# Kernel tuning notes

Hardware: AMD Instinct MI355X
Metric: run time of the kernel (lower is better)

## Reference

```python
import jax, jax.numpy as jnp
import numpy as np
from math import sqrt

EMBED = 768
HEADS = 12
EPS = 1e-12  # torch F.normalize eps


def setup_inputs() -> dict:
    key = jax.random.key(0)
    ks = jax.random.split(key, 9)
    B, N, E = 8, 4096, EMBED
    s = 1.0 / np.sqrt(E)
    x = jax.random.normal(ks[0], (B, N, E), dtype=jnp.float32)
    Wq = jax.random.normal(ks[1], (E, E), dtype=jnp.float32) * s
    bq = jnp.zeros((E,), dtype=jnp.float32)
    Wk = jax.random.normal(ks[2], (E, E), dtype=jnp.float32) * s
    bk = jnp.zeros((E,), dtype=jnp.float32)
    Wv = jax.random.normal(ks[3], (E, E), dtype=jnp.float32) * s
    bv = jnp.zeros((E,), dtype=jnp.float32)
    Wo = jax.random.normal(ks[4], (E, E), dtype=jnp.float32) * s
    bo = jnp.zeros((E,), dtype=jnp.float32)
    return {"x": x, "Wq": Wq, "bq": bq, "Wk": Wk, "bk": bk,
            "Wv": Wv, "bv": bv, "Wo": Wo, "bo": bo}


def _l2norm_tokens(t):
    # F.normalize(p=2, dim=1): normalize over the token (n) axis
    nrm = jnp.sqrt(jnp.sum(t * t, axis=1, keepdims=True))
    return t / jnp.maximum(nrm, EPS)


def reference(x, Wq, bq, Wk, bk, Wv, bv, Wo, bo):
    B, N, E = x.shape
    h = HEADS
    e = E // h
    q = (x @ Wq + bq).reshape(B, N, h, e)
    k = (x @ Wk + bk).reshape(B, N, h, e)
    v = (x @ Wv + bv).reshape(B, N, h, e)
    q = _l2norm_tokens(q)
    k = _l2norm_tokens(k)
    # cross-covariance attention over channel dim: [b, e, h, e]
    energy = jnp.einsum('bnhe,bnhq->behq', q, k)
    attn = jax.nn.softmax(energy, axis=-1) / sqrt(E)
    out = jnp.einsum('behq,bnhe->bnhq', attn, v)  # [b, n, h, e]
    out = out.reshape(B, N, E)
    return out @ Wo + bo
```

## Files before the change

### kernel.cpp

```cpp
#include <hip/hip_runtime.h>
#include <hip/hip_bf16.h>

typedef short bf16x8 __attribute__((ext_vector_type(8)));
typedef unsigned short u16x8 __attribute__((ext_vector_type(8)));
typedef unsigned short us4 __attribute__((ext_vector_type(4)));
typedef float f32x4 __attribute__((ext_vector_type(4)));
using bf16 = __hip_bfloat16;

#define EMB 768
#define NHEAD 12
#define BATCH 8
#define NTOK 4096
#define BNTOK 32768

__device__ __forceinline__ float b2f(unsigned short u) {
    union { unsigned int i; float f; } x; x.i = ((unsigned int)u) << 16; return x.f;
}
__device__ __forceinline__ unsigned short f2bu(float f) {
    bf16 h = __float2bfloat16(f);
    return *reinterpret_cast<unsigned short*>(&h);
}

__device__ __forceinline__ void gload_lds16(const void* g, void* l) {
    __builtin_amdgcn_global_load_lds(
        (const __attribute__((address_space(1))) unsigned int*)g,
        (__attribute__((address_space(3))) unsigned int*)l,
        16, 0, 0);
}

__global__ __launch_bounds__(256) void cast_x_kernel(const float* __restrict__ x,
                                                     bf16* __restrict__ xb, int n8) {
    int i = blockIdx.x * blockDim.x + threadIdx.x;
    if (i >= n8) return;
    const float4* xv = (const float4*)x;
    float4 a = xv[i * 2], b = xv[i * 2 + 1];
    u16x8 o;
    o[0] = f2bu(a.x); o[1] = f2bu(a.y); o[2] = f2bu(a.z); o[3] = f2bu(a.w);
    o[4] = f2bu(b.x); o[5] = f2bu(b.y); o[6] = f2bu(b.z); o[7] = f2bu(b.w);
    ((u16x8*)xb)[i] = o;
}

__global__ __launch_bounds__(256) void prep_w_kernel(
    const float* __restrict__ Wq, const float* __restrict__ Wk,
    const float* __restrict__ Wv, const float* __restrict__ Wo,
    const float* __restrict__ bq, const float* __restrict__ bk, const float* __restrict__ bv,
    bf16* __restrict__ WqkvT, bf16* __restrict__ WoT, float* __restrict__ bqkv) {
    const int NQKV = 2304 * 768, NO = 768 * 768;
    int i = blockIdx.x * blockDim.x + threadIdx.x;
    if (i < NQKV) {
        int nrow = i / 768, k = i % 768;
        const float* W = (nrow < 768) ? Wq : (nrow < 1536 ? Wk : Wv);
        int c = nrow % 768;
        WqkvT[i] = __float2bfloat16(W[k * 768 + c]);
    } else if (i < NQKV + NO) {
        int j = i - NQKV; int nrow = j / 768, k = j % 768;
        WoT[j] = __float2bfloat16(Wo[k * 768 + nrow]);
    } else if (i < NQKV + NO + 2304) {
        int j = i - NQKV - NO;
        bqkv[j] = (j < 768) ? bq[j] : (j < 1536 ? bk[j - 768] : bv[j - 1536]);
    }
}

template <int MODE>
__global__ __launch_bounds__(512, 1) void gemm256(
    const bf16* __restrict__ A, const bf16* __restrict__ BT,
    bf16* __restrict__ QT, bf16* __restrict__ KT, bf16* __restrict__ V,
    const float* __restrict__ bias,
    float* __restrict__ Cout, const float* __restrict__ bo) {
    __shared__ char lds[131072];
    const int NKT = 12;
    const int tid = threadIdx.x;
    const int lane = tid & 63, wid = tid >> 6;
    const int wm = wid >> 2, wn = wid & 3;
    const int lrow = lane & 15, lk = lane >> 4;

    int nwg = gridDim.x * gridDim.y;
    int bid = blockIdx.y * gridDim.x + blockIdx.x;
    int swz = (bid & 7) * (nwg >> 3) + (bid >> 3);
    int bx = swz % gridDim.x, by = swz / gridDim.x;
    const int m0 = by * 256, n0 = bx * 256;

    const bf16* bt = BT + (MODE == 1 ? (size_t)(m0 >> 12) * 589824 : 0);

    const int srow = wid * 16 + lrow;
    const int scol = ((lane >> 4) & 3) << 3;

    f32x4 acc[8][4] = {};

#define STAGE(tbuf, isb, skh, sktv) do {                                           \
    int skt_ = (sktv); if (skt_ >= NKT) skt_ = NKT - 1;                            \
    const bf16* gp_ = ((isb) ? bt + (size_t)(n0 + srow) * 768                      \
                             : A  + (size_t)(m0 + srow) * 768)                     \
                      + skt_ * 64 + (skh) * 32 + scol;                             \
    char* lp_ = lds + (tbuf) * 65536 + (isb) * 32768 + (skh) * 16384 + wid * 1024; \
    gload_lds16(gp_, lp_);                                                         \
    gload_lds16(gp_ + (size_t)128 * 768, lp_ + 8192);                              \
} while (0)

#define LOADB(cbuf, KH) do {                                                       \
    const char* bb_ = lds + (cbuf) * 65536 + 32768 + (KH) * 16384;                 \
    _Pragma("unroll") for (int ni = 0; ni < 4; ++ni)                               \
        bre[ni] = *(const bf16x8*)(bb_ + (wn * 4 + ni) * 1024 + lane * 16);        \
} while (0)

#define COMPUTE(cbuf, KH, CM) do {                                                 \
    const char* ab_ = lds + (cbuf) * 65536 + (KH) * 16384;                         \
    bf16x8 af_[4];                                                                 \
    _Pragma("unroll") for (int mi = 0; mi < 4; ++mi)                               \
        af_[mi] = *(const bf16x8*)(ab_ + (wm * 8 + (CM) * 4 + mi) * 1024 + lane * 16); \
    __builtin_amdgcn_s_setprio(1);                                                 \
    _Pragma("unroll") for (int mi = 0; mi < 4; ++mi)                               \
    _Pragma("unroll") for (int ni = 0; ni < 4; ++ni)                               \
        acc[(CM) * 4 + mi][ni] = __builtin_amdgcn_mfma_f32_16x16x32_bf16(          \
            af_[mi], bre[ni], acc[(CM) * 4 + mi][ni], 0, 0, 0);                    \
    __builtin_amdgcn_s_setprio(0);                                                 \
} while (0)

#define VMC8 asm volatile("s_waitcnt vmcnt(8)" ::: "memory")
#define BAR  __builtin_amdgcn_s_barrier()

    bf16x8 bre[4];

    STAGE(0, 0, 0, 0);
    STAGE(0, 1, 0, 0);
    STAGE(0, 0, 1, 0);
    STAGE(0, 1, 1, 0);
    STAGE(1, 0, 0, 1);
    STAGE(1, 1, 0, 1);
    VMC8; BAR;

    for (int i = 0; i < NKT; ++i) {
        const int cb = i & 1, nb = cb ^ 1;
        STAGE(nb, 0, 1, i + 1); LOADB(cb, 0); COMPUTE(cb, 0, 0); BAR;
        STAGE(nb, 1, 1, i + 1); COMPUTE(cb, 0, 1); VMC8; BAR;
        STAGE(cb, 0, 0, i + 2); LOADB(cb, 1); COMPUTE(cb, 1, 0); BAR;
        STAGE(cb, 1, 0, i + 2); COMPUTE(cb, 1, 1); VMC8; BAR;
    }

#undef STAGE
#undef LOADB
#undef COMPUTE
#undef VMC8
#undef BAR

    if (MODE == 0) {
        const int which = n0 / 768;
        if (which < 2) {
            bf16* T = (which == 0) ? QT : KT;
            const int b = m0 >> 12;
            const int tb = (m0 & 4095) + wm * 128 + lk * 4;
#pragma unroll
            for (int ri = 0; ri < 8; ++ri)
#pragma unroll
                for (int ni = 0; ni < 4; ++ni) {
                    int gcol = n0 + wn * 64 + ni * 16 + lrow;
                    int chan = gcol - which * 768;
                    float bia = bias[gcol];
                    int tokl = tb + ri * 16;
                    us4 pk;
                    pk[0] = f2bu(acc[ri][ni][0] + bia);
                    pk[1] = f2bu(acc[ri][ni][1] + bia);
                    pk[2] = f2bu(acc[ri][ni][2] + bia);
                    pk[3] = f2bu(acc[ri][ni][3] + bia);
                    *(us4*)&T[((size_t)b * 768 + chan) * 4096 + tokl] = pk;
                }
        } else {
#pragma unroll
            for (int ri = 0; ri < 8; ++ri)
#pragma unroll
                for (int ni = 0; ni < 4; ++ni) {
                    int gcol = n0 + wn * 64 + ni * 16 + lrow;
                    int chan = gcol - 1536;
                    float bia = bias[gcol];
                    size_t r0 = (size_t)(m0 + wm * 128 + ri * 16 + lk * 4);
#pragma unroll
                    for (int r = 0; r < 4; ++r)
                        V[(r0 + r) * 768 + chan] = __float2bfloat16(acc[ri][ni][r] + bia);
                }
        }
    } else {
#pragma unroll
        for (int ri = 0; ri < 8; ++ri)
#pragma unroll
            for (int ni = 0; ni < 4; ++ni) {
                int col = n0 + wn * 64 + ni * 16 + lrow;
                float bia = bo[col];
                size_t r0 = (size_t)(m0 + wm * 128 + ri * 16 + lk * 4);
#pragma unroll
                for (int r = 0; r < 4; ++r)
                    Cout[(r0 + r) * 768 + col] = acc[ri][ni][r] + bia;
            }
    }
}

__global__ __launch_bounds__(256) void gram_mfma_kernel(
    const bf16* __restrict__ QT, const bf16* __restrict__ KT,
    float* __restrict__ G, float* __restrict__ ssq, float* __restrict__ ssk) {
    const int kc = blockIdx.x, bh = blockIdx.y;
    const int b = bh / NHEAD, h = bh % NHEAD;
    const int tid = threadIdx.x, lane = tid & 63, w = tid >> 6;
    const int lrow = lane & 15, lk = lane >> 4;
    const int t0 = kc * 512 + w * 128;

    f32x4 acc[4][4] = {};
    float sqp[4] = {}, skp[4] = {};
    const size_t qbase = ((size_t)b * 768 + h * 64) * 4096;

#pragma unroll
    for (int kk = 0; kk < 4; ++kk) {
        bf16x8 a[4], bb[4];
#pragma unroll
        for (int mi = 0; mi < 4; ++mi)
            a[mi] = *(const bf16x8*)(QT + qbase + (size_t)(mi * 16 + lrow) * 4096 +
                                     t0 + kk * 32 + lk * 8);
#pragma unroll
        for (int ni = 0; ni < 4; ++ni)
            bb[ni] = *(const bf16x8*)(KT + qbase + (size_t)(ni * 16 + lrow) * 4096 +
                                      t0 + kk * 32 + lk * 8);
#pragma unroll
        for (int mi = 0; mi < 4; ++mi) {
#pragma unroll
            for (int j = 0; j < 8; ++j) {
                float qv = b2f((unsigned short)a[mi][j]);
                float kv = b2f((unsigned short)bb[mi][j]);
                sqp[mi] = fmaf(qv, qv, sqp[mi]);
                skp[mi] = fmaf(kv, kv, skp[mi]);
            }
        }
#pragma unroll
        for (int mi = 0; mi < 4; ++mi)
#pragma unroll
            for (int ni = 0; ni < 4; ++ni)
                acc[mi][ni] = __builtin_amdgcn_mfma_f32_16x16x32_bf16(a[mi], bb[ni], acc[mi][ni], 0, 0, 0);
    }

#pragma unroll
    for (int mi = 0; mi < 4; ++mi) {
        float vq = sqp[mi], vk = skp[mi];
        vq += __shfl_down(vq, 32); vq += __shfl_down(vq, 16);
        vk += __shfl_down(vk, 32); vk += __shfl_down(vk, 16);
        if (lane < 16) {
            atomicAdd(&ssq[b * 768 + h * 64 + mi * 16 + lrow], vq);
            atomicAdd(&ssk[b * 768 + h * 64 + mi * 16 + lrow], vk);
        }
    }

    float* g = G + (size_t)bh * 4096;
#pragma unroll
    for (int mi = 0; mi < 4; ++mi)
#pragma unroll
        for (int ni = 0; ni < 4; ++ni)
#pragma unroll
            for (int r = 0; r < 4; ++r) {
                int e = mi * 16 + lk * 4 + r;
                int j = ni * 16 + lrow;
                atomicAdd(&g[e * 64 + j], acc[mi][ni][r]);
            }
}

__global__ __launch_bounds__(64) void softmax_kernel(
    const float* __restrict__ G, const float* __restrict__ ssq, const float* __restrict__ ssk,
    bf16* __restrict__ attnA) {
    int bh = blockIdx.x; int b = bh / NHEAD, h = bh % NHEAD;
    int e = threadIdx.x;
    const float* g = G + (size_t)bh * 4096 + e * 64;
    float nq = fmaxf(sqrtf(ssq[b * 768 + h * 64 + e]), 1e-12f);
    float row[64];
    float mx = -1e30f;
#pragma unroll
    for (int j = 0; j < 64; ++j) {
        float nk = fmaxf(sqrtf(ssk[b * 768 + h * 64 + j]), 1e-12f);
        float en = g[j] / (nq * nk);
        row[j] = en;
        mx = fmaxf(mx, en);
    }
    float s = 0.f;
#pragma unroll
    for (int j = 0; j < 64; ++j) { row[j] = __expf(row[j] - mx); s += row[j]; }
    float inv = 0.036084391824351615f / s;
#pragma unroll
    for (int j = 0; j < 64; ++j)
        attnA[(size_t)bh * 4096 + e * 64 + j] = __float2bfloat16(row[j] * inv);
}

__global__ __launch_bounds__(256) void wtilde_kernel(
    const bf16* __restrict__ WoT, const bf16* __restrict__ attnA,
    bf16* __restrict__ WtT) {
    const int ns = blockIdx.x, bh = blockIdx.y;
    const int b = bh / NHEAD, h = bh % NHEAD;
    const int tid = threadIdx.x, lane = tid & 63, w = tid >> 6;
    const int lrow = lane & 15, lk = lane >> 4;
    const int nbase = ns * 192 + w * 48;

    f32x4 acc[3][4] = {};
#pragma unroll
    for (int kk = 0; kk < 2; ++kk) {
        bf16x8 a[3], bb[4];
#pragma unroll
        for (int mi = 0; mi < 3; ++mi)
            a[mi] = *(const bf16x8*)(WoT + (size_t)(nbase + mi * 16 + lrow) * 768 +
                                     h * 64 + kk * 32 + lk * 8);
#pragma unroll
        for (int ni = 0; ni < 4; ++ni)
            bb[ni] = *(const bf16x8*)(attnA + (size_t)bh * 4096 +
                                      (ni * 16 + lrow) * 64 + kk * 32 + lk * 8);
#pragma unroll
        for (int mi = 0; mi < 3; ++mi)
#pragma unroll
            for (int ni = 0; ni < 4; ++ni)
                acc[mi][ni] = __builtin_amdgcn_mfma_f32_16x16x32_bf16(a[mi], bb[ni], acc[mi][ni], 0, 0, 0);
    }
#pragma unroll
    for (int mi = 0; mi < 3; ++mi)
#pragma unroll
        for (int ni = 0; ni < 4; ++ni)
#pragma unroll
            for (int r = 0; r < 4; ++r) {
                int n = nbase + mi * 16 + lk * 4 + r;
                int e = ni * 16 + lrow;
                WtT[((size_t)b * 768 + n) * 768 + h * 64 + e] = __float2bfloat16(acc[mi][ni][r]);
            }
}

extern "C" void kernel_launch(void* const* d_in, const int* in_sizes, int n_in,
                              void* d_out, int out_size, void* d_ws, size_t ws_size,
                              hipStream_t stream) {
    const float* x  = (const float*)d_in[0];
    const float* Wq = (const float*)d_in[1];
    const float* bq = (const float*)d_in[2];
    const float* Wk = (const float*)d_in[3];
    const float* bk = (const float*)d_in[4];
    const float* Wv = (const float*)d_in[5];
    const float* bv = (const float*)d_in[6];
    const float* Wo = (const float*)d_in[7];
    const float* bo = (const float*)d_in[8];
    float* out = (float*)d_out;

    char* ws = (char*)d_ws;
    bf16*  xb    = (bf16*)(ws + 0);
    bf16*  WqkvT = (bf16*)(ws + 50331648);
    bf16*  WoT   = (bf16*)(ws + 53870592);
    float* bqkv  = (float*)(ws + 55050240);
    bf16*  QT    = (bf16*)(ws + 55059456);
    bf16*  KT    = (bf16*)(ws + 105391104);
    bf16*  Vb    = (bf16*)(ws + 155722752);
    float* ssq   = (float*)(ws + 206054400);
    float* ssk   = (float*)(ws + 206078976);
    float* G     = (float*)(ws + 206103552);
    bf16*  attnA = (bf16*)(ws + 207676416);
    bf16*  WtT   = xb;

    hipMemsetAsync(ws + 206054400, 0, 24576 + 24576 + 1572864, stream);

    cast_x_kernel<<<12288, 256, 0, stream>>>(x, xb, BNTOK * EMB / 8);
    prep_w_kernel<<<9225, 256, 0, stream>>>(Wq, Wk, Wv, Wo, bq, bk, bv, WqkvT, WoT, bqkv);

    gemm256<0><<<dim3(9, 128), 512, 0, stream>>>(xb, WqkvT, QT, KT, Vb, bqkv, nullptr, nullptr);

    gram_mfma_kernel<<<dim3(8, 96), 256, 0, stream>>>(QT, KT, G, ssq, ssk);
    softmax_kernel<<<96, 64, 0, stream>>>(G, ssq, ssk, attnA);
    wtilde_kernel<<<dim3(4, 96), 256, 0, stream>>>(WoT, attnA, WtT);

    gemm256<1><<<dim3(3, 128), 512, 0, stream>>>(Vb, WtT, nullptr, nullptr, nullptr, nullptr, out, bo);
}
```

Measured before the change: 357.2 us.

## Restructure GEMM main loop staging order and stage Q/K transposed epilogue through LDS

The main loop is reorganised into phases that read A and B fragments from LDS, issue the next global-to-LDS stage, then barrier, wait on LDS and run the MFMAs. It changes the prefetch order and depth (vmcnt 8 to 10, with one more stage issued in the prologue). The Q/K transposed epilogue now writes bias-added bf16 tiles into LDS and then emits 16-byte coalesced row stores, instead of scattered 8-byte stores. This trades extra barriers and LDS traffic for better memory coalescing and more load/compute overlap.

```diff
diff --git a/kernel.cpp b/kernel.cpp
--- a/kernel.cpp
+++ b/kernel.cpp
@@ -97,50 +97,53 @@
     gload_lds16(gp_ + (size_t)128 * 768, lp_ + 8192);                              \
 } while (0)
 
-#define LOADB(cbuf, KH) do {                                                       \
-    const char* bb_ = lds + (cbuf) * 65536 + 32768 + (KH) * 16384;                 \
-    _Pragma("unroll") for (int ni = 0; ni < 4; ++ni)                               \
-        bre[ni] = *(const bf16x8*)(bb_ + (wn * 4 + ni) * 1024 + lane * 16);        \
-} while (0)
-
-#define COMPUTE(cbuf, KH, CM) do {                                                 \
+#define VMC10 asm volatile("s_waitcnt vmcnt(10)" ::: "memory")
+#define BAR   __builtin_amdgcn_s_barrier()
+
+#define PH(cbuf, KH, CM, RB, STG, DOV) do {                                        \
     const char* ab_ = lds + (cbuf) * 65536 + (KH) * 16384;                         \
-    bf16x8 af_[4];                                                                 \
     _Pragma("unroll") for (int mi = 0; mi < 4; ++mi)                               \
-        af_[mi] = *(const bf16x8*)(ab_ + (wm * 8 + (CM) * 4 + mi) * 1024 + lane * 16); \
+        afr[mi] = *(const bf16x8*)(ab_ + (wm * 8 + (CM) * 4 + mi) * 1024 + lane * 16); \
+    if (RB) {                                                                      \
+        const char* bb_ = ab_ + 32768;                                             \
+        _Pragma("unroll") for (int ni = 0; ni < 4; ++ni)                           \
+            bfr[ni] = *(const bf16x8*)(bb_ + (wn * 4 + ni) * 1024 + lane * 16);    \
+    }                                                                              \
+    STG;                                                                           \
+    BAR;                                                                           \
+    asm volatile("s_waitcnt lgkmcnt(0)" ::: "memory");                             \
     __builtin_amdgcn_s_setprio(1);                                                 \
     _Pragma("unroll") for (int mi = 0; mi < 4; ++mi)                               \
     _Pragma("unroll") for (int ni = 0; ni < 4; ++ni)                               \
         acc[(CM) * 4 + mi][ni] = __builtin_amdgcn_mfma_f32_16x16x32_bf16(          \
-            af_[mi], bre[ni], acc[(CM) * 4 + mi][ni], 0, 0, 0);                    \
+            afr[mi], bfr[ni], acc[(CM) * 4 + mi][ni], 0, 0, 0);                    \
     __builtin_amdgcn_s_setprio(0);                                                 \
+    if (DOV) VMC10;                                                                \
+    BAR;                                                                           \
 } while (0)
 
-#define VMC8 asm volatile("s_waitcnt vmcnt(8)" ::: "memory")
-#define BAR  __builtin_amdgcn_s_barrier()
-
-    bf16x8 bre[4];
-
+    bf16x8 afr[4], bfr[4];
+
+    STAGE(0, 1, 0, 0);
     STAGE(0, 0, 0, 0);
-    STAGE(0, 1, 0, 0);
+    STAGE(0, 1, 1, 0);
     STAGE(0, 0, 1, 0);
-    STAGE(0, 1, 1, 0);
+    STAGE(1, 1, 0, 1);
     STAGE(1, 0, 0, 1);
-    STAGE(1, 1, 0, 1);
-    VMC8; BAR;
+    STAGE(1, 1, 1, 1);
+    VMC10; BAR;
 
     for (int i = 0; i < NKT; ++i) {
         const int cb = i & 1, nb = cb ^ 1;
-        STAGE(nb, 0, 1, i + 1); LOADB(cb, 0); COMPUTE(cb, 0, 0); BAR;
-        STAGE(nb, 1, 1, i + 1); COMPUTE(cb, 0, 1); VMC8; BAR;
-        STAGE(cb, 0, 0, i + 2); LOADB(cb, 1); COMPUTE(cb, 1, 0); BAR;
-        STAGE(cb, 1, 0, i + 2); COMPUTE(cb, 1, 1); VMC8; BAR;
+        PH(cb, 0, 0, 1, STAGE(nb, 0, 1, i + 1), 0);
+        PH(cb, 0, 1, 0, STAGE(cb, 1, 0, i + 2), 1);
+        PH(cb, 1, 0, 1, STAGE(cb, 0, 0, i + 2), 0);
+        PH(cb, 1, 1, 0, STAGE(cb, 1, 1, i + 2), 1);
     }
 
 #undef STAGE
-#undef LOADB
-#undef COMPUTE
-#undef VMC8
+#undef PH
+#undef VMC10
 #undef BAR
 
     if (MODE == 0) {
@@ -148,22 +151,39 @@
         if (which < 2) {
             bf16* T = (which == 0) ? QT : KT;
             const int b = m0 >> 12;
-            const int tb = (m0 & 4095) + wm * 128 + lk * 4;
-#pragma unroll
-            for (int ri = 0; ri < 8; ++ri)
-#pragma unroll
-                for (int ni = 0; ni < 4; ++ni) {
-                    int gcol = n0 + wn * 64 + ni * 16 + lrow;
-                    int chan = gcol - which * 768;
-                    float bia = bias[gcol];
-                    int tokl = tb + ri * 16;
-                    us4 pk;
-                    pk[0] = f2bu(acc[ri][ni][0] + bia);
-                    pk[1] = f2bu(acc[ri][ni][1] + bia);
-                    pk[2] = f2bu(acc[ri][ni][2] + bia);
-                    pk[3] = f2bu(acc[ri][ni][3] + bia);
-                    *(us4*)&T[((size_t)b * 768 + chan) * 4096 + tokl] = pk;
+            const int tok0 = m0 & 4095;
+            const int chan0 = n0 - which * 768;
+            char* eb = lds;
+            const int col = tid >> 2, q = tid & 3;
+#pragma unroll
+            for (int s = 0; s < 2; ++s) {
+                if ((wn >> 1) == s) {
+#pragma unroll
+                    for (int ri = 0; ri < 8; ++ri)
+#pragma unroll
+                        for (int ni = 0; ni < 4; ++ni) {
+                            int gcol = n0 + wn * 64 + ni * 16 + lrow;
+                            float bia = bias[gcol];
+                            int cloc = (wn & 1) * 64 + ni * 16 + lrow;
+                            int row = wm * 128 + ri * 16 + lk * 4;
+                            us4 pk;
+                            pk[0] = f2bu(acc[ri][ni][0] + bia);
+                            pk[1] = f2bu(acc[ri][ni][1] + bia);
+                            pk[2] = f2bu(acc[ri][ni][2] + bia);
+                            pk[3] = f2bu(acc[ri][ni][3] + bia);
+                            *(us4*)(eb + cloc * 528 + row * 2) = pk;
+                        }
                 }
+                __syncthreads();
+                size_t gbase = ((size_t)b * 768 + chan0 + s * 128 + col) * 4096 + tok0;
+#pragma unroll
+                for (int it = 0; it < 8; ++it) {
+                    int eo = q * 64 + it * 8;
+                    u16x8 v = *(const u16x8*)(eb + col * 528 + eo * 2);
+                    *(u16x8*)&T[gbase + eo] = v;
+                }
+                __syncthreads();
+            }
         } else {
 #pragma unroll
             for (int ri = 0; ri < 8; ++ri)
```

After: 372.4 us. 4.3% more time.

## Replace 256x256 GEMM with 128x128 tile kernel loading B directly from global

Applied to the files above, without the earlier changes.

Replaces the 512-thread 256x256 tile GEMM, which staged both A and B through 128KB of LDS, with a 256-thread 128x128 tile kernel. Only A goes through LDS (32KB, double-buffered); B fragments are read straight from global/L2 into registers. The smaller LDS and register footprint allow three blocks per CU and a larger grid, aimed at better occupancy and tail balance. In exchange, data reuse per tile drops and uncoalesced direct B loads add global traffic.

```diff
diff --git a/kernel.cpp b/kernel.cpp
--- a/kernel.cpp
+++ b/kernel.cpp
@@ -62,133 +62,122 @@
 }
 
 template <int MODE>
-__global__ __launch_bounds__(512, 1) void gemm256(
+__global__ __launch_bounds__(256, 3) void gemm128(
     const bf16* __restrict__ A, const bf16* __restrict__ BT,
     bf16* __restrict__ QT, bf16* __restrict__ KT, bf16* __restrict__ V,
     const float* __restrict__ bias,
     float* __restrict__ Cout, const float* __restrict__ bo) {
-    __shared__ char lds[131072];
+    __shared__ char lds[32768];
     const int NKT = 12;
     const int tid = threadIdx.x;
     const int lane = tid & 63, wid = tid >> 6;
-    const int wm = wid >> 2, wn = wid & 3;
+    const int wm = wid >> 1, wn = wid & 1;
     const int lrow = lane & 15, lk = lane >> 4;
 
     int nwg = gridDim.x * gridDim.y;
     int bid = blockIdx.y * gridDim.x + blockIdx.x;
     int swz = (bid & 7) * (nwg >> 3) + (bid >> 3);
     int bx = swz % gridDim.x, by = swz / gridDim.x;
-    const int m0 = by * 256, n0 = bx * 256;
-
-    const bf16* bt = BT + (MODE == 1 ? (size_t)(m0 >> 12) * 589824 : 0);
-
-    const int srow = wid * 16 + lrow;
-    const int scol = ((lane >> 4) & 3) << 3;
-
-    f32x4 acc[8][4] = {};
-
-#define STAGE(tbuf, isb, skh, sktv) do {                                           \
-    int skt_ = (sktv); if (skt_ >= NKT) skt_ = NKT - 1;                            \
-    const bf16* gp_ = ((isb) ? bt + (size_t)(n0 + srow) * 768                      \
-                             : A  + (size_t)(m0 + srow) * 768)                     \
-                      + skt_ * 64 + (skh) * 32 + scol;                             \
-    char* lp_ = lds + (tbuf) * 65536 + (isb) * 32768 + (skh) * 16384 + wid * 1024; \
-    gload_lds16(gp_, lp_);                                                         \
-    gload_lds16(gp_ + (size_t)128 * 768, lp_ + 8192);                              \
+    const int m0 = by * 128, n0 = bx * 128;
+
+    const bf16* Ab = A + (size_t)m0 * 768;
+    const bf16* btp = BT + (MODE == 1 ? (size_t)(m0 >> 12) * 589824 : 0) + (size_t)n0 * 768;
+
+    f32x4 acc[4][4] = {};
+    bf16x8 afr[8], bfr[8];
+
+#define STAGE(tbuf, sktv) do {                                                     \
+    int skt_ = (sktv); if (skt_ > NKT - 1) skt_ = NKT - 1;                         \
+    _Pragma("unroll") for (int g = 0; g < 4; ++g) {                                \
+        int fid_ = g * 4 + wid;                                                    \
+        const bf16* gp_ = Ab + (size_t)((fid_ >> 1) * 16 + lrow) * 768 +           \
+                          skt_ * 64 + (fid_ & 1) * 32 + lk * 8;                    \
+        gload_lds16(gp_, lds + (tbuf) * 16384 + g * 4096 + tid * 16);              \
+    }                                                                              \
 } while (0)
 
-#define LOADB(cbuf, KH) do {                                                       \
-    const char* bb_ = lds + (cbuf) * 65536 + 32768 + (KH) * 16384;                 \
-    _Pragma("unroll") for (int ni = 0; ni < 4; ++ni)                               \
-        bre[ni] = *(const bf16x8*)(bb_ + (wn * 4 + ni) * 1024 + lane * 16);        \
-} while (0)
-
-#define COMPUTE(cbuf, KH, CM) do {                                                 \
-    const char* ab_ = lds + (cbuf) * 65536 + (KH) * 16384;                         \
-    bf16x8 af_[4];                                                                 \
-    _Pragma("unroll") for (int mi = 0; mi < 4; ++mi)                               \
-        af_[mi] = *(const bf16x8*)(ab_ + (wm * 8 + (CM) * 4 + mi) * 1024 + lane * 16); \
-    __builtin_amdgcn_s_setprio(1);                                                 \
-    _Pragma("unroll") for (int mi = 0; mi < 4; ++mi)                               \
-    _Pragma("unroll") for (int ni = 0; ni < 4; ++ni)                               \
-        acc[(CM) * 4 + mi][ni] = __builtin_amdgcn_mfma_f32_16x16x32_bf16(          \
-            af_[mi], bre[ni], acc[(CM) * 4 + mi][ni], 0, 0, 0);                    \
-    __builtin_amdgcn_s_setprio(0);                                                 \
-} while (0)
-
-#define VMC8 asm volatile("s_waitcnt vmcnt(8)" ::: "memory")
-#define BAR  __builtin_amdgcn_s_barrier()
-
-    bf16x8 bre[4];
-
-    STAGE(0, 0, 0, 0);
-    STAGE(0, 1, 0, 0);
-    STAGE(0, 0, 1, 0);
-    STAGE(0, 1, 1, 0);
-    STAGE(1, 0, 0, 1);
-    STAGE(1, 1, 0, 1);
-    VMC8; BAR;
+    STAGE(0, 0);
 
     for (int i = 0; i < NKT; ++i) {
         const int cb = i & 1, nb = cb ^ 1;
-        STAGE(nb, 0, 1, i + 1); LOADB(cb, 0); COMPUTE(cb, 0, 0); BAR;
-        STAGE(nb, 1, 1, i + 1); COMPUTE(cb, 0, 1); VMC8; BAR;
-        STAGE(cb, 0, 0, i + 2); LOADB(cb, 1); COMPUTE(cb, 1, 0); BAR;
-        STAGE(cb, 1, 0, i + 2); COMPUTE(cb, 1, 1); VMC8; BAR;
-    }
-
+        STAGE(nb, i + 1);
+#pragma unroll
+        for (int kh = 0; kh < 2; ++kh)
+#pragma unroll
+            for (int ni = 0; ni < 4; ++ni)
+                bfr[kh * 4 + ni] = *(const bf16x8*)(btp +
+                    (size_t)(wn * 64 + ni * 16 + lrow) * 768 + i * 64 + kh * 32 + lk * 8);
+        asm volatile("s_waitcnt vmcnt(12)" ::: "memory");
+        __builtin_amdgcn_s_barrier();
+#pragma unroll
+        for (int kh = 0; kh < 2; ++kh)
+#pragma unroll
+            for (int mi = 0; mi < 4; ++mi)
+                afr[kh * 4 + mi] = *(const bf16x8*)(lds + cb * 16384 +
+                    ((wm * 4 + mi) * 2 + kh) * 1024 + lane * 16);
+        asm volatile("s_waitcnt vmcnt(4)" ::: "memory");
+        asm volatile("s_waitcnt lgkmcnt(0)" ::: "memory");
+        __builtin_amdgcn_sched_barrier(0);
+        __builtin_amdgcn_s_setprio(1);
+#pragma unroll
+        for (int kh = 0; kh < 2; ++kh)
+#pragma unroll
+            for (int mi = 0; mi < 4; ++mi)
+#pragma unroll
+                for (int ni = 0; ni < 4; ++ni)
+                    acc[mi][ni] = __builtin_amdgcn_mfma_f32_16x16x32_bf16(
+                        afr[kh * 4 + mi], bfr[kh * 4 + ni], acc[mi][ni], 0, 0, 0);
+        __builtin_amdgcn_s_setprio(0);
+        __builtin_amdgcn_s_barrier();
+    }
 #undef STAGE
-#undef LOADB
-#undef COMPUTE
-#undef VMC8
-#undef BAR
 
     if (MODE == 0) {
         const int which = n0 / 768;
+        const int cb0 = n0 - which * 768 + wn * 64;
         if (which < 2) {
             bf16* T = (which == 0) ? QT : KT;
             const int b = m0 >> 12;
-            const int tb = (m0 & 4095) + wm * 128 + lk * 4;
-#pragma unroll
-            for (int ri = 0; ri < 8; ++ri)
+            const int tb = (m0 & 4095) + wm * 64 + lk * 4;
+#pragma unroll
+            for (int mi = 0; mi < 4; ++mi)
 #pragma unroll
                 for (int ni = 0; ni < 4; ++ni) {
                     int gcol = n0 + wn * 64 + ni * 16 + lrow;
-                    int chan = gcol - which * 768;
+                    int chan = cb0 + ni * 16 + lrow;
                     float bia = bias[gcol];
-                    int tokl = tb + ri * 16;
                     us4 pk;
-                    pk[0] = f2bu(acc[ri][ni][0] + bia);
-                    pk[1] = f2bu(acc[ri][ni][1] + bia);
-                    pk[2] = f2bu(acc[ri][ni][2] + bia);
-                    pk[3] = f2bu(acc[ri][ni][3] + bia);
-                    *(us4*)&T[((size_t)b * 768 + chan) * 4096 + tokl] = pk;
+                    pk[0] = f2bu(acc[mi][ni][0] + bia);
+                    pk[1] = f2bu(acc[mi][ni][1] + bia);
+                    pk[2] = f2bu(acc[mi][ni][2] + bia);
+                    pk[3] = f2bu(acc[mi][ni][3] + bia);
+                    *(us4*)&T[((size_t)b * 768 + chan) * 4096 + tb + mi * 16] = pk;
                 }
         } else {
 #pragma unroll
-            for (int ri = 0; ri < 8; ++ri)
+            for (int mi = 0; mi < 4; ++mi)
 #pragma unroll
                 for (int ni = 0; ni < 4; ++ni) {
                     int gcol = n0 + wn * 64 + ni * 16 + lrow;
-                    int chan = gcol - 1536;
+                    int chan = cb0 + ni * 16 + lrow;
                     float bia = bias[gcol];
-                    size_t r0 = (size_t)(m0 + wm * 128 + ri * 16 + lk * 4);
+                    size_t r0 = (size_t)(m0 + wm * 64 + mi * 16 + lk * 4);
 #pragma unroll
                     for (int r = 0; r < 4; ++r)
-                        V[(r0 + r) * 768 + chan] = __float2bfloat16(acc[ri][ni][r] + bia);
+                        V[(r0 + r) * 768 + chan] = __float2bfloat16(acc[mi][ni][r] + bia);
                 }
         }
     } else {
 #pragma unroll
-        for (int ri = 0; ri < 8; ++ri)
+        for (int mi = 0; mi < 4; ++mi)
 #pragma unroll
             for (int ni = 0; ni < 4; ++ni) {
                 int col = n0 + wn * 64 + ni * 16 + lrow;
                 float bia = bo[col];
-                size_t r0 = (size_t)(m0 + wm * 128 + ri * 16 + lk * 4);
+                size_t r0 = (size_t)(m0 + wm * 64 + mi * 16 + lk * 4);
 #pragma unroll
                 for (int r = 0; r < 4; ++r)
-                    Cout[(r0 + r) * 768 + col] = acc[ri][ni][r] + bia;
+                    Cout[(r0 + r) * 768 + col] = acc[mi][ni][r] + bia;
             }
     }
 }
@@ -355,11 +344,11 @@
     cast_x_kernel<<<12288, 256, 0, stream>>>(x, xb, BNTOK * EMB / 8);
     prep_w_kernel<<<9225, 256, 0, stream>>>(Wq, Wk, Wv, Wo, bq, bk, bv, WqkvT, WoT, bqkv);
 
-    gemm256<0><<<dim3(9, 128), 512, 0, stream>>>(xb, WqkvT, QT, KT, Vb, bqkv, nullptr, nullptr);
+    gemm128<0><<<dim3(18, 256), 256, 0, stream>>>(xb, WqkvT, QT, KT, Vb, bqkv, nullptr, nullptr);
 
     gram_mfma_kernel<<<dim3(8, 96), 256, 0, stream>>>(QT, KT, G, ssq, ssk);
     softmax_kernel<<<96, 64, 0, stream>>>(G, ssq, ssk, attnA);
     wtilde_kernel<<<dim3(4, 96), 256, 0, stream>>>(WoT, attnA, WtT);
 
-    gemm256<1><<<dim3(3, 128), 512, 0, stream>>>(Vb, WtT, nullptr, nullptr, nullptr, nullptr, out, bo);
-}
+    gemm128<1><<<dim3(6, 256), 256, 0, stream>>>(Vb, WtT, nullptr, nullptr, nullptr, nullptr, out, bo);
+}
```

New measurement: 561.7 us. 1.57x slower.
